# Kernel optimization log

Measured on AMD Instinct MI355X. Metric: run time of the kernel, lower is better.

The kernel has to match this reference:

```python
import jax, jax.numpy as jnp
import numpy as np

P = 3; C = 64; IMG = 48; G = IMG // P
D = C * P * P          # 576 embedding dim == flatten dim
NH = 12; HD = D // NH  # 48 head dim
HID = 4 * D            # 2304
NL = 4; S = G * G      # 256 patches
NQ = 6
QN, QP = -8.0, 7.0     # 4-bit signed LSQ range
EPS = 1e-5


def lsq(w):
    # LSQ fake-quant of weights, step size from LSQ init formula, STE rounding
    alpha = 2.0 * jnp.mean(jnp.abs(w)) / jnp.sqrt(QP)
    q = jnp.clip(w / alpha, QN, QP)
    q = q + jax.lax.stop_gradient(jnp.round(q) - q)
    return q * alpha


def qlinear(x, w, b=None):
    y = x @ lsq(w).T
    return y if b is None else y + b


def ln(x, g, b):
    m = jnp.mean(x, -1, keepdims=True)
    v = jnp.var(x, -1, keepdims=True)
    return (x - m) / jnp.sqrt(v + EPS) * g + b


def mha(q, k, v, in_w, out_w):
    # q,k,v: [S,B,D]; in_w: [3D,D]; out_w: [D,D]; no biases
    Wq, Wk, Wv = jnp.split(lsq(in_w), 3, axis=0)
    def heads(t, W):
        return (t @ W.T).reshape(t.shape[0], t.shape[1], NH, HD)
    qh = heads(q, Wq) * (1.0 / jnp.sqrt(HD))
    kh = heads(k, Wk)
    vh = heads(v, Wv)
    att = jax.nn.softmax(jnp.einsum('qbhd,kbhd->bhqk', qh, kh), axis=-1)
    o = jnp.einsum('bhqk,kbhd->qbhd', att, vh).reshape(q.shape[0], q.shape[1], D)
    return o @ lsq(out_w).T


def _forward(x, lin_enc_w, lin_enc_b, pos_emb, query_embed_w,
             enc_in_w, enc_out_w, enc_l1_w, enc_l1_b, enc_l2_w, enc_l2_b,
             enc_ln1_g, enc_ln1_b, enc_ln2_g, enc_ln2_b,
             dec_sa_in_w, dec_sa_out_w, dec_ca_in_w, dec_ca_out_w,
             dec_l1_w, dec_l1_b, dec_l2_w, dec_l2_b,
             dec_ln1_g, dec_ln1_b, dec_ln2_g, dec_ln2_b, dec_ln3_g, dec_ln3_b,
             head1_w, head1_b, head2_w, head2_b, query_idx):
    B = x.shape[0]
    # unfold -> [S,B,flat], channel-major patch flattening like F.unfold
    t = x.reshape(B, C, G, P, G, P).transpose(0, 1, 3, 5, 2, 4)
    t = t.reshape(B, C * P * P, G * G).transpose(2, 0, 1)  # [S,B,D]
    t = qlinear(t, lin_enc_w, lin_enc_b) + t
    qe = query_embed_w[query_idx].reshape(S, 1, D)   # query_pos, broadcasts over B
    pos = pos_emb[:, None, :]                        # [S,1,D]
    h = t + pos
    for l in range(NL):  # encoder (pre-norm)
        h2 = ln(h, enc_ln1_g[l], enc_ln1_b[l])
        h = h + mha(h2, h2, h2, enc_in_w[l], enc_out_w[l])
        h2 = ln(h, enc_ln2_g[l], enc_ln2_b[l])
        h = h + qlinear(jax.nn.relu(qlinear(h2, enc_l1_w[l], enc_l1_b[l])), enc_l2_w[l], enc_l2_b[l])
    mem = h
    o = mem
    for l in range(NL):  # decoder, memory = encoder output
        o2 = ln(o, dec_ln1_g[l], dec_ln1_b[l])
        qk = o2 + qe
        o = o + mha(qk, qk, o2, dec_sa_in_w[l], dec_sa_out_w[l])
        o2 = ln(o, dec_ln2_g[l], dec_ln2_b[l])
        o = o + mha(o2 + qe, mem, mem, dec_ca_in_w[l], dec_ca_out_w[l])
        o2 = ln(o, dec_ln3_g[l], dec_ln3_b[l])
        o = o + qlinear(jax.nn.relu(qlinear(o2, dec_l1_w[l], dec_l1_b[l])), dec_l2_w[l], dec_l2_b[l])
    # mlp_head with residual
    o = o + qlinear(jax.nn.relu(qlinear(o, head1_w, head1_b)), head2_w, head2_b)
    # fold back: [S,B,D] -> [B,C,IMG,IMG]
    y = o.transpose(1, 2, 0).reshape(B, C, P, P, G, G).transpose(0, 1, 4, 2, 5, 3)
    return y.reshape(B, C, IMG, IMG)


def setup_inputs() -> dict:
    key = jax.random.key(0)
    ks = iter(jax.random.split(key, 64))
    def w(shape):
        return jax.random.normal(next(ks), shape, jnp.float32) * 0.02
    B = 4
    inp = {
        'x': jax.random.normal(next(ks), (B, C, IMG, IMG), jnp.float32),
        'lin_enc_w': w((D, D)), 'lin_enc_b': jnp.zeros((D,), jnp.float32),
        'pos_emb': w((S, D)),
        'query_embed_w': w((NQ, S * D)),
        'enc_in_w': w((NL, 3 * D, D)), 'enc_out_w': w((NL, D, D)),
        'enc_l1_w': w((NL, HID, D)), 'enc_l1_b': jnp.zeros((NL, HID), jnp.float32),
        'enc_l2_w': w((NL, D, HID)), 'enc_l2_b': jnp.zeros((NL, D), jnp.float32),
        'enc_ln1_g': jnp.ones((NL, D), jnp.float32), 'enc_ln1_b': jnp.zeros((NL, D), jnp.float32),
        'enc_ln2_g': jnp.ones((NL, D), jnp.float32), 'enc_ln2_b': jnp.zeros((NL, D), jnp.float32),
        'dec_sa_in_w': w((NL, 3 * D, D)), 'dec_sa_out_w': w((NL, D, D)),
        'dec_ca_in_w': w((NL, 3 * D, D)), 'dec_ca_out_w': w((NL, D, D)),
        'dec_l1_w': w((NL, HID, D)), 'dec_l1_b': jnp.zeros((NL, HID), jnp.float32),
        'dec_l2_w': w((NL, D, HID)), 'dec_l2_b': jnp.zeros((NL, D), jnp.float32),
        'dec_ln1_g': jnp.ones((NL, D), jnp.float32), 'dec_ln1_b': jnp.zeros((NL, D), jnp.float32),
        'dec_ln2_g': jnp.ones((NL, D), jnp.float32), 'dec_ln2_b': jnp.zeros((NL, D), jnp.float32),
        'dec_ln3_g': jnp.ones((NL, D), jnp.float32), 'dec_ln3_b': jnp.zeros((NL, D), jnp.float32),
        'head1_w': w((HID, D)), 'head1_b': jnp.zeros((HID,), jnp.float32),
        'head2_w': w((D, HID)), 'head2_b': jnp.zeros((D,), jnp.float32),
        'query_idx': 0,
    }
    return inp


def reference(x, lin_enc_w, lin_enc_b, pos_emb, query_embed_w,
              enc_in_w, enc_out_w, enc_l1_w, enc_l1_b, enc_l2_w, enc_l2_b,
              enc_ln1_g, enc_ln1_b, enc_ln2_g, enc_ln2_b,
              dec_sa_in_w, dec_sa_out_w, dec_ca_in_w, dec_ca_out_w,
              dec_l1_w, dec_l1_b, dec_l2_w, dec_l2_b,
              dec_ln1_g, dec_ln1_b, dec_ln2_g, dec_ln2_b, dec_ln3_g, dec_ln3_b,
              head1_w, head1_b, head2_w, head2_b, query_idx):
    return _forward(x, lin_enc_w, lin_enc_b, pos_emb, query_embed_w,
                    enc_in_w, enc_out_w, enc_l1_w, enc_l1_b, enc_l2_w, enc_l2_b,
                    enc_ln1_g, enc_ln1_b, enc_ln2_g, enc_ln2_b,
                    dec_sa_in_w, dec_sa_out_w, dec_ca_in_w, dec_ca_out_w,
                    dec_l1_w, dec_l1_b, dec_l2_w, dec_l2_b,
                    dec_ln1_g, dec_ln1_b, dec_ln2_g, dec_ln2_b, dec_ln3_g, dec_ln3_b,
                    head1_w, head1_b, head2_w, head2_b, query_idx)
```

## Files before the change

kernel.cpp:

```cpp
#include <hip/hip_runtime.h>
#include <cstddef>

#define Pp    3
#define Cc    64
#define IMGi  48
#define Gg    16
#define Dd    576
#define NHh   12
#define HDd   48
#define HIDh  2304
#define NLl   4
#define Ss    256
#define Bb    4
#define Mm    1024
#define EPSf  1e-5f
#define NJOBS 43
#define NSTAT 20

typedef short short8 __attribute__((ext_vector_type(8)));
typedef short short4v __attribute__((ext_vector_type(4)));
typedef float f32x4  __attribute__((ext_vector_type(4)));

struct QJobs { const float* ptr[NJOBS]; int n[NJOBS]; int off[NJOBS]; };

__device__ __forceinline__ short f2bf(float f) {
  unsigned u = __float_as_uint(f);
  u = u + 0x7fffu + ((u >> 16) & 1u);
  return (short)(u >> 16);
}

typedef __attribute__((address_space(3))) unsigned lds_u32;
typedef __attribute__((address_space(1))) const unsigned glob_u32;
__device__ __forceinline__ void gload_lds16(const void* g, void* l) {
  __builtin_amdgcn_global_load_lds((glob_u32*)g, (lds_u32*)l, 16, 0, 0);
}


__global__ void k_zero(float* p, int n) {
  int i = blockIdx.x * blockDim.x + threadIdx.x;
  if (i < n) p[i] = 0.f;
}

__global__ void k_abssum(QJobs jobs, float* absum) {
  int job = blockIdx.x >> 6, blk = blockIdx.x & 63;
  const float4* p4 = (const float4*)jobs.ptr[job];
  int n4 = jobs.n[job] >> 2;
  float s0 = 0.f, s1 = 0.f, s2 = 0.f, s3 = 0.f;
  for (int i = blk * 1024 + threadIdx.x; i < n4; i += 64 * 1024) {
    float4 v = p4[i];
    s0 += fabsf(v.x) + fabsf(v.y) + fabsf(v.z) + fabsf(v.w);
    int i1 = i + 256;
    if (i1 < n4) { float4 w = p4[i1]; s1 += fabsf(w.x) + fabsf(w.y) + fabsf(w.z) + fabsf(w.w); }
    int i2 = i + 512;
    if (i2 < n4) { float4 w = p4[i2]; s2 += fabsf(w.x) + fabsf(w.y) + fabsf(w.z) + fabsf(w.w); }
    int i3 = i + 768;
    if (i3 < n4) { float4 w = p4[i3]; s3 += fabsf(w.x) + fabsf(w.y) + fabsf(w.z) + fabsf(w.w); }
  }
  float s = (s0 + s1) + (s2 + s3);
  #pragma unroll
  for (int o = 32; o; o >>= 1) s += __shfl_xor(s, o);
  __shared__ float red[4];
  if ((threadIdx.x & 63) == 0) red[threadIdx.x >> 6] = s;
  __syncthreads();
  if (threadIdx.x == 0) atomicAdd(&absum[job], (red[0] + red[1]) + (red[2] + red[3]));
}

__global__ void k_alpha(QJobs jobs, const float* absum, float* alpha, float* inva) {
  int j = threadIdx.x;
  if (j < NJOBS) {
    float a = 2.f * (absum[j] / (float)jobs.n[j]) / sqrtf(7.f);
    alpha[j] = a;
    inva[j] = 1.f / a;
  }
}

__global__ void k_quant(QJobs jobs, const float* __restrict__ inva, short* __restrict__ wq) {
  int job = blockIdx.x >> 7, blk = blockIdx.x & 127;
  const float* p = jobs.ptr[job];
  int n8 = jobs.n[job] >> 3;
  short* dst = wq + (size_t)jobs.off[job];
  float ia = inva[job];
  for (int i = blk * 512 + threadIdx.x; i < n8; i += 128 * 512) {
    const float4* p4 = (const float4*)(p + (size_t)i * 8);
    float4 w0 = p4[0], w1 = p4[1];
    int i1 = i + 256;
    float4 w2, w3;
    bool has2 = i1 < n8;
    if (has2) { const float4* q4 = (const float4*)(p + (size_t)i1 * 8); w2 = q4[0]; w3 = q4[1]; }
    short8 bv;
    bv[0] = f2bf(rintf(fminf(7.f, fmaxf(-8.f, w0.x * ia))));
    bv[1] = f2bf(rintf(fminf(7.f, fmaxf(-8.f, w0.y * ia))));
    bv[2] = f2bf(rintf(fminf(7.f, fmaxf(-8.f, w0.z * ia))));
    bv[3] = f2bf(rintf(fminf(7.f, fmaxf(-8.f, w0.w * ia))));
    bv[4] = f2bf(rintf(fminf(7.f, fmaxf(-8.f, w1.x * ia))));
    bv[5] = f2bf(rintf(fminf(7.f, fmaxf(-8.f, w1.y * ia))));
    bv[6] = f2bf(rintf(fminf(7.f, fmaxf(-8.f, w1.z * ia))));
    bv[7] = f2bf(rintf(fminf(7.f, fmaxf(-8.f, w1.w * ia))));
    *(short8*)(dst + (size_t)i * 8) = bv;
    if (has2) {
      short8 cv;
      cv[0] = f2bf(rintf(fminf(7.f, fmaxf(-8.f, w2.x * ia))));
      cv[1] = f2bf(rintf(fminf(7.f, fmaxf(-8.f, w2.y * ia))));
      cv[2] = f2bf(rintf(fminf(7.f, fmaxf(-8.f, w2.z * ia))));
      cv[3] = f2bf(rintf(fminf(7.f, fmaxf(-8.f, w2.w * ia))));
      cv[4] = f2bf(rintf(fminf(7.f, fmaxf(-8.f, w3.x * ia))));
      cv[5] = f2bf(rintf(fminf(7.f, fmaxf(-8.f, w3.y * ia))));
      cv[6] = f2bf(rintf(fminf(7.f, fmaxf(-8.f, w3.z * ia))));
      cv[7] = f2bf(rintf(fminf(7.f, fmaxf(-8.f, w3.w * ia))));
      *(short8*)(dst + (size_t)i1 * 8) = cv;
    }
  }
}

__global__ void k_patchify(const float* __restrict__ x, float* __restrict__ t) {
  int i = blockIdx.x * 256 + threadIdx.x;
  if (i >= Mm * Dd) return;
  int d = i % Dd, row = i / Dd;
  int b = row % Bb, s = row / Bb;
  int c = d / 9, r = d % 9;
  int p1 = r / 3, p2 = r % 3;
  int g1 = s / Gg, g2 = s % Gg;
  t[i] = x[((size_t)(b * Cc + c) * IMGi + (g1 * Pp + p1)) * IMGi + (g2 * Pp + p2)];
}

__global__ void k_unpatch(const float* __restrict__ h, float* __restrict__ out) {
  int i = blockIdx.x * 256 + threadIdx.x;
  if (i >= Bb * Cc * IMGi * IMGi) return;
  int j = i % IMGi, t = i / IMGi;
  int r = t % IMGi; t /= IMGi;
  int c = t % Cc;
  int b = t / Cc;
  int g1 = r / Pp, p1 = r % Pp, g2 = j / Pp, p2 = j % Pp;
  int s = g1 * Gg + g2;
  int d = c * 9 + p1 * 3 + p2;
  out[i] = h[(size_t)(s * Bb + b) * Dd + d];
}

#define MT 64
#define NT 64
#define KC 288
#define LDKA 296
#define LDKB 304
#define BCHUNKS 38

__device__ __forceinline__ int bswz(int row, int colByte) {
  return row * (LDKB * 2) + (colByte ^ (((row >> 2) & 3) << 4));
}

__global__ __launch_bounds__(256)
void k_gemm_mfma(const float* __restrict__ Xa, const float* __restrict__ Xb,
                 int n_split, int ldx,
                 const float* __restrict__ qe, const int* __restrict__ qidx,
                 const float* __restrict__ lng, const float* __restrict__ lnb,
                 const float* __restrict__ statA, const float* __restrict__ statB,
                 const float* __restrict__ Wraw, const short* __restrict__ Wq,
                 const float* __restrict__ bias, const float* __restrict__ pos,
                 const float* res, int ldr,
                 float* out, int ldo, float* out2, float* statOut,
                 int N, int K,
                 const float* __restrict__ alpha_p, const float* __restrict__ inva_p,
                 int slot, int relu)
{
  __shared__ short As[MT][LDKA];
  __shared__ short Bs[NT * LDKB];
  const int tid  = threadIdx.x;
  const int wave = tid >> 6, lane = tid & 63;
  const int quad = lane >> 4, l15 = lane & 15;
  const int tile_m = blockIdx.y * MT, tile_n = blockIdx.x * NT;
  const int m_off = (wave >> 1) * 32, n_off = (wave & 1) * 32;
  const int sr = tid >> 2;
  const int sc = (tid & 3) * 8;
  const float inva = inva_p[slot];

  const bool isA = (!Xb || tile_n < n_split);
  const float* X = isA ? Xa : Xb;
  const bool addqe = (qe != nullptr) && isA;
  const float* stat = isA ? statA : statB;
  size_t qe_off = 0;
  if (addqe) qe_off = (size_t)qidx[0] * ((size_t)Ss * Dd);

  float mean = 0.f, sinv = 1.f;
  if (stat) {
    float2 st = *(const float2*)&stat[2 * (tile_m + sr)];
    mean = st.x * (1.f / (float)Dd);
    float var = st.y * (1.f / (float)Dd) - mean * mean;
    sinv = rsqrtf(var + EPSf);
  }

  f32x4 acc00 = {0,0,0,0}, acc01 = {0,0,0,0}, acc10 = {0,0,0,0}, acc11 = {0,0,0,0};

  for (int kc = 0; kc < K; kc += KC) {
    if (Wq) {
      #pragma unroll
      for (int j = 0; j < 10; ++j) {
        const int c = wave * 10 + j;
        if (c < BCHUNKS) {
          const int p = c * 512 + lane * 8;
          const int prow = p / LDKB;
          const int pcolB = (p % LDKB) * 2;
          const int lcolB = pcolB ^ (((prow >> 2) & 3) << 4);
          const short* src = (lcolB < 576)
            ? Wq + (size_t)(tile_n + prow) * K + kc + (lcolB >> 1)
            : Wq;
          gload_lds16(src, (char*)Bs + c * 1024);
        }
      }
    } else {
      const float* wr = Wraw + (size_t)(tile_n + sr) * K + kc;
      #pragma unroll
      for (int j = 0; j < 9; ++j) {
        const int k = sc + j * 32;
        float4 w0 = *(const float4*)(wr + k);
        float4 w1 = *(const float4*)(wr + k + 4);
        short8 bv;
        bv[0] = f2bf(rintf(fminf(7.f, fmaxf(-8.f, w0.x * inva))));
        bv[1] = f2bf(rintf(fminf(7.f, fmaxf(-8.f, w0.y * inva))));
        bv[2] = f2bf(rintf(fminf(7.f, fmaxf(-8.f, w0.z * inva))));
        bv[3] = f2bf(rintf(fminf(7.f, fmaxf(-8.f, w0.w * inva))));
        bv[4] = f2bf(rintf(fminf(7.f, fmaxf(-8.f, w1.x * inva))));
        bv[5] = f2bf(rintf(fminf(7.f, fmaxf(-8.f, w1.y * inva))));
        bv[6] = f2bf(rintf(fminf(7.f, fmaxf(-8.f, w1.z * inva))));
        bv[7] = f2bf(rintf(fminf(7.f, fmaxf(-8.f, w1.w * inva))));
        *(short8*)((char*)Bs + bswz(sr, k * 2)) = bv;
      }
    }

    {
      const int arow = tile_m + sr;
      const float* ar = X + (size_t)arow * ldx + kc;
      const float* qr = addqe ? (qe + qe_off + (size_t)(arow >> 2) * Dd + kc) : nullptr;
      #pragma unroll
      for (int j = 0; j < 9; ++j) {
        const int k = sc + j * 32;
        float4 a0 = *(const float4*)(ar + k);
        float4 a1 = *(const float4*)(ar + k + 4);
        if (stat) {
          float4 g0 = *(const float4*)(lng + kc + k);
          float4 g1 = *(const float4*)(lng + kc + k + 4);
          float4 b0 = *(const float4*)(lnb + kc + k);
          float4 b1 = *(const float4*)(lnb + kc + k + 4);
          a0.x = (a0.x - mean) * sinv * g0.x + b0.x;
          a0.y = (a0.y - mean) * sinv * g0.y + b0.y;
          a0.z = (a0.z - mean) * sinv * g0.z + b0.z;
          a0.w = (a0.w - mean) * sinv * g0.w + b0.w;
          a1.x = (a1.x - mean) * sinv * g1.x + b1.x;
          a1.y = (a1.y - mean) * sinv * g1.y + b1.y;
          a1.z = (a1.z - mean) * sinv * g1.z + b1.z;
          a1.w = (a1.w - mean) * sinv * g1.w + b1.w;
        }
        if (addqe) {
          float4 q0 = *(const float4*)(qr + k);
          float4 q1 = *(const float4*)(qr + k + 4);
          a0.x += q0.x; a0.y += q0.y; a0.z += q0.z; a0.w += q0.w;
          a1.x += q1.x; a1.y += q1.y; a1.z += q1.z; a1.w += q1.w;
        }
        short8 av;
        av[0] = f2bf(a0.x); av[1] = f2bf(a0.y); av[2] = f2bf(a0.z); av[3] = f2bf(a0.w);
        av[4] = f2bf(a1.x); av[5] = f2bf(a1.y); av[6] = f2bf(a1.z); av[7] = f2bf(a1.w);
        *(short8*)&As[sr][k] = av;
      }
    }
    __syncthreads();

    #pragma unroll 3
    for (int ks = 0; ks < KC / 32; ++ks) {
      const int kb = ks * 32 + quad * 8;
      short8 af0 = *(short8*)&As[m_off + l15][kb];
      short8 af1 = *(short8*)&As[m_off + 16 + l15][kb];
      short8 bf0 = *(const short8*)((const char*)Bs + bswz(n_off + l15, kb * 2));
      short8 bf1 = *(const short8*)((const char*)Bs + bswz(n_off + 16 + l15, kb * 2));
      acc00 = __builtin_amdgcn_mfma_f32_16x16x32_bf16(af0, bf0, acc00, 0, 0, 0);
      acc01 = __builtin_amdgcn_mfma_f32_16x16x32_bf16(af0, bf1, acc01, 0, 0, 0);
      acc10 = __builtin_amdgcn_mfma_f32_16x16x32_bf16(af1, bf0, acc10, 0, 0, 0);
      acc11 = __builtin_amdgcn_mfma_f32_16x16x32_bf16(af1, bf1, acc11, 0, 0, 0);
    }
    __syncthreads();
  }

  const float a_s = alpha_p[slot];
  const int rowb = tile_m + m_off + quad * 4;
  const int colb = tile_n + n_off + l15;
  f32x4 accs[4] = {acc00, acc01, acc10, acc11};
  float vsum[2][4], vsq[2][4];
  #pragma unroll
  for (int rt = 0; rt < 2; ++rt)
    #pragma unroll
    for (int r = 0; r < 4; ++r) { vsum[rt][r] = 0.f; vsq[rt][r] = 0.f; }

  #pragma unroll
  for (int t = 0; t < 4; ++t) {
    int row0 = rowb + ((t >> 1) * 16);
    int col  = colb + ((t & 1) * 16);
    float bv = bias ? bias[col] : 0.f;
    #pragma unroll
    for (int r = 0; r < 4; ++r) {
      int row = row0 + r;
      float v = accs[t][r] * a_s + bv;
      if (res) v += res[(size_t)row * ldr + col];
      if (pos) v += pos[(size_t)(row >> 2) * Dd + col];
      if (relu) v = fmaxf(v, 0.f);
      out[(size_t)row * ldo + col] = v;
      if (out2) out2[(size_t)row * ldo + col] = v;
      vsum[t >> 1][r] += v;
      vsq[t >> 1][r]  += v * v;
    }
  }

  if (statOut) {
    #pragma unroll
    for (int rt = 0; rt < 2; ++rt) {
      #pragma unroll
      for (int r = 0; r < 4; ++r) {
        float s = vsum[rt][r], q = vsq[rt][r];
        #pragma unroll
        for (int o = 1; o < 16; o <<= 1) {
          s += __shfl_xor(s, o);
          q += __shfl_xor(q, o);
        }
        if (l15 == 0) {
          int row = rowb + rt * 16 + r;
          atomicAdd(&statOut[2 * row],     s);
          atomicAdd(&statOut[2 * row + 1], q);
        }
      }
    }
  }
}

__global__ __launch_bounds__(256)
void k_attn(const float* __restrict__ QKV, float* __restrict__ ctx, float scale) {
  __shared__ short Ks[256][72];
  __shared__ short Qs[64][72];
  __shared__ short Vt[48][264];
  __shared__ short Pq[64][264];
  const int qt = blockIdx.x;
  const int b  = blockIdx.y / NHh, h = blockIdx.y % NHh;
  const int tid = threadIdx.x;
  const int w = tid >> 6, lane = tid & 63, quad = lane >> 4, l15 = lane & 15;

  {
    const float* kp = QKV + (size_t)(tid * Bb + b) * 1728 + Dd + h * HDd;
    #pragma unroll
    for (int d0 = 0; d0 < 48; d0 += 4) {
      float4 f = *(const float4*)(kp + d0);
      short4v v = { f2bf(f.x), f2bf(f.y), f2bf(f.z), f2bf(f.w) };
      *(short4v*)&Ks[tid][d0] = v;
    }
    short4v z = {0, 0, 0, 0};
    *(short4v*)&Ks[tid][48] = z; *(short4v*)&Ks[tid][52] = z;
    *(short4v*)&Ks[tid][56] = z; *(short4v*)&Ks[tid][60] = z;
    const float* vp = QKV + (size_t)(tid * Bb + b) * 1728 + 2 * Dd + h * HDd;
    #pragma unroll
    for (int d0 = 0; d0 < 48; d0 += 4) {
      float4 f = *(const float4*)(vp + d0);
      Vt[d0 + 0][tid] = f2bf(f.x);
      Vt[d0 + 1][tid] = f2bf(f.y);
      Vt[d0 + 2][tid] = f2bf(f.z);
      Vt[d0 + 3][tid] = f2bf(f.w);
    }
    if (tid < 64) {
      const float* qp = QKV + (size_t)((qt * 64 + tid) * Bb + b) * 1728 + h * HDd;
      #pragma unroll
      for (int d0 = 0; d0 < 48; d0 += 4) {
        float4 f = *(const float4*)(qp + d0);
        short4v v = { f2bf(f.x), f2bf(f.y), f2bf(f.z), f2bf(f.w) };
        *(short4v*)&Qs[tid][d0] = v;
      }
      *(short4v*)&Qs[tid][48] = z; *(short4v*)&Qs[tid][52] = z;
      *(short4v*)&Qs[tid][56] = z; *(short4v*)&Qs[tid][60] = z;
    }
  }
  __syncthreads();

  short8 bq0 = *(short8*)&Qs[w * 16 + l15][quad * 8];
  short8 bq1 = *(short8*)&Qs[w * 16 + l15][32 + quad * 8];
  f32x4 sf[16];
  #pragma unroll
  for (int mt = 0; mt < 16; ++mt) {
    f32x4 acc = {0, 0, 0, 0};
    short8 a0 = *(short8*)&Ks[mt * 16 + l15][quad * 8];
    short8 a1 = *(short8*)&Ks[mt * 16 + l15][32 + quad * 8];
    acc = __builtin_amdgcn_mfma_f32_16x16x32_bf16(a0, bq0, acc, 0, 0, 0);
    acc = __builtin_amdgcn_mfma_f32_16x16x32_bf16(a1, bq1, acc, 0, 0, 0);
    sf[mt] = acc;
  }

  float mx = -1e30f;
  #pragma unroll
  for (int mt = 0; mt < 16; ++mt)
    #pragma unroll
    for (int r = 0; r < 4; ++r) {
      sf[mt][r] *= scale;
      mx = fmaxf(mx, sf[mt][r]);
    }
  mx = fmaxf(mx, __shfl_xor(mx, 16));
  mx = fmaxf(mx, __shfl_xor(mx, 32));
  float sum = 0.f;
  #pragma unroll
  for (int mt = 0; mt < 16; ++mt)
    #pragma unroll
    for (int r = 0; r < 4; ++r) {
      float e = __expf(sf[mt][r] - mx);
      sf[mt][r] = e;
      sum += e;
    }
  sum += __shfl_xor(sum, 16);
  sum += __shfl_xor(sum, 32);
  float inv = 1.f / sum;

  #pragma unroll
  for (int mt = 0; mt < 16; ++mt) {
    short4v p = { f2bf(sf[mt][0] * inv), f2bf(sf[mt][1] * inv),
                  f2bf(sf[mt][2] * inv), f2bf(sf[mt][3] * inv) };
    *(short4v*)&Pq[w * 16 + l15][mt * 16 + quad * 4] = p;
  }
  __syncthreads();

  f32x4 of0 = {0,0,0,0}, of1 = {0,0,0,0}, of2 = {0,0,0,0};
  #pragma unroll
  for (int kt = 0; kt < 8; ++kt) {
    short8 a = *(short8*)&Pq[w * 16 + l15][kt * 32 + quad * 8];
    short8 b0 = *(short8*)&Vt[l15][kt * 32 + quad * 8];
    short8 b1 = *(short8*)&Vt[16 + l15][kt * 32 + quad * 8];
    short8 b2 = *(short8*)&Vt[32 + l15][kt * 32 + quad * 8];
    of0 = __builtin_amdgcn_mfma_f32_16x16x32_bf16(a, b0, of0, 0, 0, 0);
    of1 = __builtin_amdgcn_mfma_f32_16x16x32_bf16(a, b1, of1, 0, 0, 0);
    of2 = __builtin_amdgcn_mfma_f32_16x16x32_bf16(a, b2, of2, 0, 0, 0);
  }
  const int qg = qt * 64 + w * 16 + quad * 4;
  #pragma unroll
  for (int r = 0; r < 4; ++r) {
    float* cr = ctx + (size_t)((qg + r) * Bb + b) * Dd + h * HDd + l15;
    cr[0]  = of0[r];
    cr[16] = of1[r];
    cr[32] = of2[r];
  }
}


extern "C" void kernel_launch(void* const* d_in, const int* in_sizes, int n_in,
                              void* d_out, int out_size, void* d_ws, size_t ws_size,
                              hipStream_t stream) {
  (void)in_sizes; (void)n_in; (void)out_size;
  const float* x            = (const float*)d_in[0];
  const float* lin_enc_w    = (const float*)d_in[1];
  const float* lin_enc_b    = (const float*)d_in[2];
  const float* pos_emb      = (const float*)d_in[3];
  const float* query_embed  = (const float*)d_in[4];
  const float* enc_in_w     = (const float*)d_in[5];
  const float* enc_out_w    = (const float*)d_in[6];
  const float* enc_l1_w     = (const float*)d_in[7];
  const float* enc_l1_b     = (const float*)d_in[8];
  const float* enc_l2_w     = (const float*)d_in[9];
  const float* enc_l2_b     = (const float*)d_in[10];
  const float* enc_ln1_g    = (const float*)d_in[11];
  const float* enc_ln1_b    = (const float*)d_in[12];
  const float* enc_ln2_g    = (const float*)d_in[13];
  const float* enc_ln2_b    = (const float*)d_in[14];
  const float* dec_sa_in_w  = (const float*)d_in[15];
  const float* dec_sa_out_w = (const float*)d_in[16];
  const float* dec_ca_in_w  = (const float*)d_in[17];
  const float* dec_ca_out_w = (const float*)d_in[18];
  const float* dec_l1_w     = (const float*)d_in[19];
  const float* dec_l1_b     = (const float*)d_in[20];
  const float* dec_l2_w     = (const float*)d_in[21];
  const float* dec_l2_b     = (const float*)d_in[22];
  const float* dec_ln1_g    = (const float*)d_in[23];
  const float* dec_ln1_b    = (const float*)d_in[24];
  const float* dec_ln2_g    = (const float*)d_in[25];
  const float* dec_ln2_b    = (const float*)d_in[26];
  const float* dec_ln3_g    = (const float*)d_in[27];
  const float* dec_ln3_b    = (const float*)d_in[28];
  const float* head1_w      = (const float*)d_in[29];
  const float* head1_b      = (const float*)d_in[30];
  const float* head2_w      = (const float*)d_in[31];
  const float* head2_b      = (const float*)d_in[32];
  const int*   query_idx    = (const int*)d_in[33];
  float* out = (float*)d_out;

  const int DD  = Dd * Dd;
  const int IN3 = 3 * Dd * Dd;
  const int FF  = HIDh * Dd;
  const int MD  = Mm * Dd;

  float* ws = (float*)d_ws;
  float* ABSUM = ws;
  float* ALPHA = ws + 64;
  float* INVA  = ws + 128;
  float* STAT  = ws + 256;
  const int STATF = NSTAT * Mm * 2;
  float* H   = STAT + STATF;
  float* MEM = H   + MD;
  float* SCR = MEM + MD;
  float* CTX = SCR + MD;
  float* QKV = CTX + MD;
  size_t act_floats = 256 + (size_t)STATF + 4 * (size_t)MD + (size_t)Mm * HIDh;
  short* WQ = (short*)(ws + act_floats);
  const size_t WQ_ELEMS = (size_t)DD + 4 * ((size_t)IN3 + DD + FF + FF)
                        + 4 * ((size_t)IN3 + DD + IN3 + DD + FF + FF)
                        + 2 * (size_t)FF;
  const bool use_wq = ws_size >= act_floats * 4 + WQ_ELEMS * 2;

  auto T = [&](int i) { return STAT + (size_t)i * (Mm * 2); };

  QJobs jobs;
  int j = 0; int off = 0;
  auto addjob = [&](const float* p, int n) { jobs.ptr[j] = p; jobs.n[j] = n; jobs.off[j] = off; off += n; j++; };
  addjob(lin_enc_w, DD);
  for (int l = 0; l < NLl; ++l) addjob(enc_in_w  + (size_t)l * IN3, IN3);
  for (int l = 0; l < NLl; ++l) addjob(enc_out_w + (size_t)l * DD,  DD);
  for (int l = 0; l < NLl; ++l) addjob(enc_l1_w  + (size_t)l * FF,  FF);
  for (int l = 0; l < NLl; ++l) addjob(enc_l2_w  + (size_t)l * FF,  FF);
  for (int l = 0; l < NLl; ++l) addjob(dec_sa_in_w  + (size_t)l * IN3, IN3);
  for (int l = 0; l < NLl; ++l) addjob(dec_sa_out_w + (size_t)l * DD,  DD);
  for (int l = 0; l < NLl; ++l) addjob(dec_ca_in_w  + (size_t)l * IN3, IN3);
  for (int l = 0; l < NLl; ++l) addjob(dec_ca_out_w + (size_t)l * DD,  DD);
  for (int l = 0; l < NLl; ++l) addjob(dec_l1_w + (size_t)l * FF, FF);
  for (int l = 0; l < NLl; ++l) addjob(dec_l2_w + (size_t)l * FF, FF);
  addjob(head1_w, FF);
  addjob(head2_w, FF);

  const int ZN = 256 + STATF;
  k_zero<<<(ZN + 255) / 256, 256, 0, stream>>>(ws, ZN);
  k_abssum<<<NJOBS * 64, 256, 0, stream>>>(jobs, ABSUM);
  k_alpha<<<1, 64, 0, stream>>>(jobs, ABSUM, ALPHA, INVA);
  if (use_wq) k_quant<<<NJOBS * 128, 256, 0, stream>>>(jobs, INVA, WQ);

  auto gemm = [&](const float* Xa, const float* Xb, int n_split, int ldx,
                  const float* qe, const float* lng, const float* lnb,
                  const float* statA, const float* statB,
                  const float* W, int slot, const float* bias, const float* pos,
                  const float* res, int ldr,
                  float* o, int ldo, float* o2, float* statOut,
                  int N, int K, int relu) {
    dim3 grid(N / NT, Mm / MT);
    const short* wq = use_wq ? WQ + (size_t)jobs.off[slot] : nullptr;
    const float* wr = use_wq ? nullptr : W;
    k_gemm_mfma<<<grid, 256, 0, stream>>>(Xa, Xb, n_split, ldx, qe, query_idx,
                                          lng, lnb, statA, statB,
                                          wr, wq, bias, pos, res, ldr,
                                          o, ldo, o2, statOut,
                                          N, K, ALPHA, INVA, slot, relu);
  };

  const float scale = 1.f / sqrtf((float)HDd);
  auto attn = [&](const float* out_w, int out_slot, float* statOut) {
    k_attn<<<dim3(Ss / 64, Bb * NHh), 256, 0, stream>>>(QKV, CTX, scale);
    gemm(CTX, nullptr, 0, Dd, nullptr, nullptr, nullptr, nullptr, nullptr,
         out_w, out_slot, nullptr, nullptr, H, Dd, H, Dd, nullptr, statOut,
         Dd, Dd, 0);
  };

  const int NELEM = Mm * Dd;
  const int EB = (NELEM + 255) / 256;

  k_patchify<<<EB, 256, 0, stream>>>(x, SCR);
  gemm(SCR, nullptr, 0, Dd, nullptr, nullptr, nullptr, nullptr, nullptr,
       lin_enc_w, 0, lin_enc_b, pos_emb, SCR, Dd, H, Dd, nullptr, T(0),
       Dd, Dd, 0);

  for (int l = 0; l < NLl; ++l) {
    gemm(H, nullptr, 0, Dd, nullptr, enc_ln1_g + l * Dd, enc_ln1_b + l * Dd,
         T(2 * l), nullptr,
         enc_in_w + (size_t)l * IN3, 1 + l,
         nullptr, nullptr, nullptr, 0, QKV, 1728, nullptr, nullptr, 1728, Dd, 0);
    attn(enc_out_w + (size_t)l * DD, 5 + l, T(2 * l + 1));
    gemm(H, nullptr, 0, Dd, nullptr, enc_ln2_g + l * Dd, enc_ln2_b + l * Dd,
         T(2 * l + 1), nullptr,
         enc_l1_w + (size_t)l * FF, 9 + l,
         enc_l1_b + l * HIDh, nullptr, nullptr, 0, QKV, HIDh, nullptr, nullptr,
         HIDh, Dd, 1);
    gemm(QKV, nullptr, 0, HIDh, nullptr, nullptr, nullptr, nullptr, nullptr,
         enc_l2_w + (size_t)l * FF, 13 + l,
         enc_l2_b + l * Dd, nullptr, H, Dd, H, Dd,
         (l == NLl - 1) ? MEM : nullptr, T(2 * l + 2), Dd, HIDh, 0);
  }

  for (int l = 0; l < NLl; ++l) {
    float* ln1s = T(8 + 3 * l);
    gemm(H, H, 2 * Dd, Dd, query_embed,
         dec_ln1_g + l * Dd, dec_ln1_b + l * Dd, ln1s, ln1s,
         dec_sa_in_w + (size_t)l * IN3, 17 + l,
         nullptr, nullptr, nullptr, 0, QKV, 1728, nullptr, nullptr, 1728, Dd, 0);
    attn(dec_sa_out_w + (size_t)l * DD, 21 + l, T(9 + 3 * l));
    gemm(H, MEM, Dd, Dd, query_embed,
         dec_ln2_g + l * Dd, dec_ln2_b + l * Dd, T(9 + 3 * l), nullptr,
         dec_ca_in_w + (size_t)l * IN3, 25 + l,
         nullptr, nullptr, nullptr, 0, QKV, 1728, nullptr, nullptr, 1728, Dd, 0);
    attn(dec_ca_out_w + (size_t)l * DD, 29 + l, T(10 + 3 * l));
    gemm(H, nullptr, 0, Dd, nullptr, dec_ln3_g + l * Dd, dec_ln3_b + l * Dd,
         T(10 + 3 * l), nullptr,
         dec_l1_w + (size_t)l * FF, 33 + l,
         dec_l1_b + l * HIDh, nullptr, nullptr, 0, QKV, HIDh, nullptr, nullptr,
         HIDh, Dd, 1);
    gemm(QKV, nullptr, 0, HIDh, nullptr, nullptr, nullptr, nullptr, nullptr,
         dec_l2_w + (size_t)l * FF, 37 + l,
         dec_l2_b + l * Dd, nullptr, H, Dd, H, Dd, nullptr,
         (l < NLl - 1) ? T(11 + 3 * l) : nullptr, Dd, HIDh, 0);
  }

  gemm(H, nullptr, 0, Dd, nullptr, nullptr, nullptr, nullptr, nullptr,
       head1_w, 41, head1_b, nullptr, nullptr, 0, QKV, HIDh, nullptr, nullptr,
       HIDh, Dd, 1);
  gemm(QKV, nullptr, 0, HIDh, nullptr, nullptr, nullptr, nullptr, nullptr,
       head2_w, 42, head2_b, nullptr, H, Dd, H, Dd, nullptr, nullptr,
       Dd, HIDh, 0);

  k_unpatch<<<EB, 256, 0, stream>>>(H, out);
}
```

Measured before the change: 1.531 ms.

## Store intermediate activations in bf16 and stage GEMM A-tiles asynchronously into LDS

Activations consumed as GEMM inputs (hidden state, QKV, FFN hidden, attention context, encoder memory) are now written in bf16 alongside or instead of fp32. This halves the global traffic for these buffers and removes the per-element fp32-to-bf16 conversion in the GEMM A-load and in attention staging. When no LayerNorm or query-embedding add is needed, the A tile is loaded with direct global-to-LDS async copies using the same swizzled layout as B. Residual paths keep fp32 copies, but LayerNorm inputs are now read from bf16, which adds rounding error before normalization.

After: 1.330 ms. 1.15x faster.

```diff
diff --git a/kernel.cpp b/kernel.cpp
--- a/kernel.cpp
+++ b/kernel.cpp
@@ -20,6 +20,7 @@
 typedef short short8 __attribute__((ext_vector_type(8)));
 typedef short short4v __attribute__((ext_vector_type(4)));
 typedef float f32x4  __attribute__((ext_vector_type(4)));
+typedef unsigned short ushort_t;
 
 struct QJobs { const float* ptr[NJOBS]; int n[NJOBS]; int off[NJOBS]; };
 
@@ -27,6 +28,9 @@
   unsigned u = __float_as_uint(f);
   u = u + 0x7fffu + ((u >> 16) & 1u);
   return (short)(u >> 16);
+}
+__device__ __forceinline__ float bf2f(short s) {
+  return __uint_as_float(((unsigned)(unsigned short)s) << 16);
 }
 
 typedef __attribute__((address_space(3))) unsigned lds_u32;
@@ -112,7 +116,8 @@
   }
 }
 
-__global__ void k_patchify(const float* __restrict__ x, float* __restrict__ t) {
+__global__ void k_patchify(const float* __restrict__ x, float* __restrict__ t,
+                           ushort_t* __restrict__ tb) {
   int i = blockIdx.x * 256 + threadIdx.x;
   if (i >= Mm * Dd) return;
   int d = i % Dd, row = i / Dd;
@@ -120,7 +125,9 @@
   int c = d / 9, r = d % 9;
   int p1 = r / 3, p2 = r % 3;
   int g1 = s / Gg, g2 = s % Gg;
-  t[i] = x[((size_t)(b * Cc + c) * IMGi + (g1 * Pp + p1)) * IMGi + (g2 * Pp + p2)];
+  float v = x[((size_t)(b * Cc + c) * IMGi + (g1 * Pp + p1)) * IMGi + (g2 * Pp + p2)];
+  t[i] = v;
+  tb[i] = (ushort_t)f2bf(v);
 }
 
 __global__ void k_unpatch(const float* __restrict__ h, float* __restrict__ out) {
@@ -139,7 +146,6 @@
 #define MT 64
 #define NT 64
 #define KC 288
-#define LDKA 296
 #define LDKB 304
 #define BCHUNKS 38
 
@@ -147,8 +153,26 @@
   return row * (LDKB * 2) + (colByte ^ (((row >> 2) & 3) << 4));
 }
 
+__device__ __forceinline__ void stage_async(const ushort_t* base, int ld,
+                                            char* lds, int wave, int lane) {
+  #pragma unroll
+  for (int j = 0; j < 10; ++j) {
+    const int c = wave * 10 + j;
+    if (c < BCHUNKS) {
+      const int p = c * 512 + lane * 8;
+      const int prow = p / LDKB;
+      const int pcol2 = (p % LDKB) * 2;
+      const int lcol = pcol2 ^ (((prow >> 2) & 3) << 4);
+      const ushort_t* src = (lcol < 576)
+        ? base + (size_t)prow * ld + (lcol >> 1)
+        : base;
+      gload_lds16(src, lds + c * 1024);
+    }
+  }
+}
+
 __global__ __launch_bounds__(256)
-void k_gemm_mfma(const float* __restrict__ Xa, const float* __restrict__ Xb,
+void k_gemm_mfma(const ushort_t* __restrict__ Xa, const ushort_t* __restrict__ Xb,
                  int n_split, int ldx,
                  const float* __restrict__ qe, const int* __restrict__ qidx,
                  const float* __restrict__ lng, const float* __restrict__ lnb,
@@ -156,12 +180,13 @@
                  const float* __restrict__ Wraw, const short* __restrict__ Wq,
                  const float* __restrict__ bias, const float* __restrict__ pos,
                  const float* res, int ldr,
-                 float* out, int ldo, float* out2, float* statOut,
+                 float* out, int ldo,
+                 ushort_t* outbf, ushort_t* outbf2, float* statOut,
                  int N, int K,
                  const float* __restrict__ alpha_p, const float* __restrict__ inva_p,
                  int slot, int relu)
 {
-  __shared__ short As[MT][LDKA];
+  __shared__ short As[NT * LDKB];
   __shared__ short Bs[NT * LDKB];
   const int tid  = threadIdx.x;
   const int wave = tid >> 6, lane = tid & 63;
@@ -173,9 +198,10 @@
   const float inva = inva_p[slot];
 
   const bool isA = (!Xb || tile_n < n_split);
-  const float* X = isA ? Xa : Xb;
+  const ushort_t* X = isA ? Xa : Xb;
   const bool addqe = (qe != nullptr) && isA;
   const float* stat = isA ? statA : statB;
+  const bool a_reg = (stat != nullptr) || addqe;
   size_t qe_off = 0;
   if (addqe) qe_off = (size_t)qidx[0] * ((size_t)Ss * Dd);
 
@@ -191,20 +217,8 @@
 
   for (int kc = 0; kc < K; kc += KC) {
     if (Wq) {
-      #pragma unroll
-      for (int j = 0; j < 10; ++j) {
-        const int c = wave * 10 + j;
-        if (c < BCHUNKS) {
-          const int p = c * 512 + lane * 8;
-          const int prow = p / LDKB;
-          const int pcolB = (p % LDKB) * 2;
-          const int lcolB = pcolB ^ (((prow >> 2) & 3) << 4);
-          const short* src = (lcolB < 576)
-            ? Wq + (size_t)(tile_n + prow) * K + kc + (lcolB >> 1)
-            : Wq;
-          gload_lds16(src, (char*)Bs + c * 1024);
-        }
-      }
+      stage_async((const ushort_t*)Wq + (size_t)tile_n * K + kc, K,
+                  (char*)Bs, wave, lane);
     } else {
       const float* wr = Wraw + (size_t)(tile_n + sr) * K + kc;
       #pragma unroll
@@ -225,39 +239,43 @@
       }
     }
 
-    {
+    if (!a_reg) {
+      stage_async(X + (size_t)tile_m * ldx + kc, ldx, (char*)As, wave, lane);
+    } else {
       const int arow = tile_m + sr;
-      const float* ar = X + (size_t)arow * ldx + kc;
+      const ushort_t* xr = X + (size_t)arow * ldx + kc;
       const float* qr = addqe ? (qe + qe_off + (size_t)(arow >> 2) * Dd + kc) : nullptr;
       #pragma unroll
       for (int j = 0; j < 9; ++j) {
         const int k = sc + j * 32;
-        float4 a0 = *(const float4*)(ar + k);
-        float4 a1 = *(const float4*)(ar + k + 4);
+        short8 xv = *(const short8*)(xr + k);
+        float a[8];
+        #pragma unroll
+        for (int e = 0; e < 8; ++e) a[e] = bf2f(xv[e]);
         if (stat) {
           float4 g0 = *(const float4*)(lng + kc + k);
           float4 g1 = *(const float4*)(lng + kc + k + 4);
           float4 b0 = *(const float4*)(lnb + kc + k);
           float4 b1 = *(const float4*)(lnb + kc + k + 4);
-          a0.x = (a0.x - mean) * sinv * g0.x + b0.x;
-          a0.y = (a0.y - mean) * sinv * g0.y + b0.y;
-          a0.z = (a0.z - mean) * sinv * g0.z + b0.z;
-          a0.w = (a0.w - mean) * sinv * g0.w + b0.w;
-          a1.x = (a1.x - mean) * sinv * g1.x + b1.x;
-          a1.y = (a1.y - mean) * sinv * g1.y + b1.y;
-          a1.z = (a1.z - mean) * sinv * g1.z + b1.z;
-          a1.w = (a1.w - mean) * sinv * g1.w + b1.w;
+          a[0] = (a[0] - mean) * sinv * g0.x + b0.x;
+          a[1] = (a[1] - mean) * sinv * g0.y + b0.y;
+          a[2] = (a[2] - mean) * sinv * g0.z + b0.z;
+          a[3] = (a[3] - mean) * sinv * g0.w + b0.w;
+          a[4] = (a[4] - mean) * sinv * g1.x + b1.x;
+          a[5] = (a[5] - mean) * sinv * g1.y + b1.y;
+          a[6] = (a[6] - mean) * sinv * g1.z + b1.z;
+          a[7] = (a[7] - mean) * sinv * g1.w + b1.w;
         }
         if (addqe) {
           float4 q0 = *(const float4*)(qr + k);
           float4 q1 = *(const float4*)(qr + k + 4);
-          a0.x += q0.x; a0.y += q0.y; a0.z += q0.z; a0.w += q0.w;
-          a1.x += q1.x; a1.y += q1.y; a1.z += q1.z; a1.w += q1.w;
+          a[0] += q0.x; a[1] += q0.y; a[2] += q0.z; a[3] += q0.w;
+          a[4] += q1.x; a[5] += q1.y; a[6] += q1.z; a[7] += q1.w;
         }
         short8 av;
-        av[0] = f2bf(a0.x); av[1] = f2bf(a0.y); av[2] = f2bf(a0.z); av[3] = f2bf(a0.w);
-        av[4] = f2bf(a1.x); av[5] = f2bf(a1.y); av[6] = f2bf(a1.z); av[7] = f2bf(a1.w);
-        *(short8*)&As[sr][k] = av;
+        #pragma unroll
+        for (int e = 0; e < 8; ++e) av[e] = f2bf(a[e]);
+        *(short8*)((char*)As + bswz(sr, k * 2)) = av;
       }
     }
     __syncthreads();
@@ -265,8 +283,8 @@
     #pragma unroll 3
     for (int ks = 0; ks < KC / 32; ++ks) {
       const int kb = ks * 32 + quad * 8;
-      short8 af0 = *(short8*)&As[m_off + l15][kb];
-      short8 af1 = *(short8*)&As[m_off + 16 + l15][kb];
+      short8 af0 = *(const short8*)((const char*)As + bswz(m_off + l15, kb * 2));
+      short8 af1 = *(const short8*)((const char*)As + bswz(m_off + 16 + l15, kb * 2));
       short8 bf0 = *(const short8*)((const char*)Bs + bswz(n_off + l15, kb * 2));
       short8 bf1 = *(const short8*)((const char*)Bs + bswz(n_off + 16 + l15, kb * 2));
       acc00 = __builtin_amdgcn_mfma_f32_16x16x32_bf16(af0, bf0, acc00, 0, 0, 0);
@@ -299,8 +317,9 @@
       if (res) v += res[(size_t)row * ldr + col];
       if (pos) v += pos[(size_t)(row >> 2) * Dd + col];
       if (relu) v = fmaxf(v, 0.f);
-      out[(size_t)row * ldo + col] = v;
-      if (out2) out2[(size_t)row * ldo + col] = v;
+      if (out)    out[(size_t)row * ldo + col] = v;
+      if (outbf)  outbf[(size_t)row * ldo + col]  = (ushort_t)f2bf(v);
+      if (outbf2) outbf2[(size_t)row * ldo + col] = (ushort_t)f2bf(v);
       vsum[t >> 1][r] += v;
       vsq[t >> 1][r]  += v * v;
     }
@@ -328,7 +347,7 @@
 }
 
 __global__ __launch_bounds__(256)
-void k_attn(const float* __restrict__ QKV, float* __restrict__ ctx, float scale) {
+void k_attn(const ushort_t* __restrict__ QKV, ushort_t* __restrict__ ctx, float scale) {
   __shared__ short Ks[256][72];
   __shared__ short Qs[64][72];
   __shared__ short Vt[48][264];
@@ -339,33 +358,25 @@
   const int w = tid >> 6, lane = tid & 63, quad = lane >> 4, l15 = lane & 15;
 
   {
-    const float* kp = QKV + (size_t)(tid * Bb + b) * 1728 + Dd + h * HDd;
+    const ushort_t* kp = QKV + (size_t)(tid * Bb + b) * 1728 + Dd + h * HDd;
     #pragma unroll
-    for (int d0 = 0; d0 < 48; d0 += 4) {
-      float4 f = *(const float4*)(kp + d0);
-      short4v v = { f2bf(f.x), f2bf(f.y), f2bf(f.z), f2bf(f.w) };
-      *(short4v*)&Ks[tid][d0] = v;
-    }
+    for (int d0 = 0; d0 < 48; d0 += 8)
+      *(short8*)&Ks[tid][d0] = *(const short8*)(kp + d0);
     short4v z = {0, 0, 0, 0};
     *(short4v*)&Ks[tid][48] = z; *(short4v*)&Ks[tid][52] = z;
     *(short4v*)&Ks[tid][56] = z; *(short4v*)&Ks[tid][60] = z;
-    const float* vp = QKV + (size_t)(tid * Bb + b) * 1728 + 2 * Dd + h * HDd;
+    const ushort_t* vp = QKV + (size_t)(tid * Bb + b) * 1728 + 2 * Dd + h * HDd;
     #pragma unroll
-    for (int d0 = 0; d0 < 48; d0 += 4) {
-      float4 f = *(const float4*)(vp + d0);
-      Vt[d0 + 0][tid] = f2bf(f.x);
-      Vt[d0 + 1][tid] = f2bf(f.y);
-      Vt[d0 + 2][tid] = f2bf(f.z);
-      Vt[d0 + 3][tid] = f2bf(f.w);
+    for (int d0 = 0; d0 < 48; d0 += 8) {
+      short8 v = *(const short8*)(vp + d0);
+      #pragma unroll
+      for (int e = 0; e < 8; ++e) Vt[d0 + e][tid] = v[e];
     }
     if (tid < 64) {
-      const float* qp = QKV + (size_t)((qt * 64 + tid) * Bb + b) * 1728 + h * HDd;
+      const ushort_t* qp = QKV + (size_t)((qt * 64 + tid) * Bb + b) * 1728 + h * HDd;
       #pragma unroll
-      for (int d0 = 0; d0 < 48; d0 += 4) {
-        float4 f = *(const float4*)(qp + d0);
-        short4v v = { f2bf(f.x), f2bf(f.y), f2bf(f.z), f2bf(f.w) };
-        *(short4v*)&Qs[tid][d0] = v;
-      }
+      for (int d0 = 0; d0 < 48; d0 += 8)
+        *(short8*)&Qs[tid][d0] = *(const short8*)(qp + d0);
       *(short4v*)&Qs[tid][48] = z; *(short4v*)&Qs[tid][52] = z;
       *(short4v*)&Qs[tid][56] = z; *(short4v*)&Qs[tid][60] = z;
     }
@@ -430,10 +441,10 @@
   const int qg = qt * 64 + w * 16 + quad * 4;
   #pragma unroll
   for (int r = 0; r < 4; ++r) {
-    float* cr = ctx + (size_t)((qg + r) * Bb + b) * Dd + h * HDd + l15;
-    cr[0]  = of0[r];
-    cr[16] = of1[r];
-    cr[32] = of2[r];
+    ushort_t* cr = ctx + (size_t)((qg + r) * Bb + b) * Dd + h * HDd + l15;
+    cr[0]  = (ushort_t)f2bf(of0[r]);
+    cr[16] = (ushort_t)f2bf(of1[r]);
+    cr[32] = (ushort_t)f2bf(of2[r]);
   }
 }
 
@@ -490,16 +501,19 @@
   float* STAT  = ws + 256;
   const int STATF = NSTAT * Mm * 2;
   float* H   = STAT + STATF;
-  float* MEM = H   + MD;
-  float* SCR = MEM + MD;
-  float* CTX = SCR + MD;
-  float* QKV = CTX + MD;
-  size_t act_floats = 256 + (size_t)STATF + 4 * (size_t)MD + (size_t)Mm * HIDh;
-  short* WQ = (short*)(ws + act_floats);
+  float* SCR = H + MD;
+  ushort_t* Hb   = (ushort_t*)(SCR + MD);
+  ushort_t* SCRb = Hb + MD;
+  ushort_t* MEMb = SCRb + MD;
+  ushort_t* CTXb = MEMb + MD;
+  ushort_t* QKVb = CTXb + MD;
+  size_t act_bytes = (256 + (size_t)STATF + 2 * (size_t)MD) * 4
+                   + (4 * (size_t)MD + (size_t)Mm * HIDh) * 2;
+  short* WQ = (short*)(QKVb + (size_t)Mm * HIDh);
   const size_t WQ_ELEMS = (size_t)DD + 4 * ((size_t)IN3 + DD + FF + FF)
                         + 4 * ((size_t)IN3 + DD + IN3 + DD + FF + FF)
                         + 2 * (size_t)FF;
-  const bool use_wq = ws_size >= act_floats * 4 + WQ_ELEMS * 2;
+  const bool use_wq = ws_size >= act_bytes + WQ_ELEMS * 2;
 
   auto T = [&](int i) { return STAT + (size_t)i * (Mm * 2); };
 
@@ -526,85 +540,90 @@
   k_alpha<<<1, 64, 0, stream>>>(jobs, ABSUM, ALPHA, INVA);
   if (use_wq) k_quant<<<NJOBS * 128, 256, 0, stream>>>(jobs, INVA, WQ);
 
-  auto gemm = [&](const float* Xa, const float* Xb, int n_split, int ldx,
+  auto gemm = [&](const ushort_t* Xa, const ushort_t* Xb, int n_split, int ldx,
                   const float* qe, const float* lng, const float* lnb,
                   const float* statA, const float* statB,
                   const float* W, int slot, const float* bias, const float* pos,
                   const float* res, int ldr,
-                  float* o, int ldo, float* o2, float* statOut,
-                  int N, int K, int relu) {
+                  float* o, int ldo, ushort_t* obf, ushort_t* obf2,
+                  float* statOut, int N, int K, int relu) {
     dim3 grid(N / NT, Mm / MT);
     const short* wq = use_wq ? WQ + (size_t)jobs.off[slot] : nullptr;
     const float* wr = use_wq ? nullptr : W;
     k_gemm_mfma<<<grid, 256, 0, stream>>>(Xa, Xb, n_split, ldx, qe, query_idx,
                                           lng, lnb, statA, statB,
                                           wr, wq, bias, pos, res, ldr,
-                                          o, ldo, o2, statOut,
+                                          o, ldo, obf, obf2, statOut,
                                           N, K, ALPHA, INVA, slot, relu);
   };
 
   const float scale = 1.f / sqrtf((float)HDd);
   auto attn = [&](const float* out_w, int out_slot, float* statOut) {
-    k_attn<<<dim3(Ss / 64, Bb * NHh), 256, 0, stream>>>(QKV, CTX, scale);
-    gemm(CTX, nullptr, 0, Dd, nullptr, nullptr, nullptr, nullptr, nullptr,
-         out_w, out_slot, nullptr, nullptr, H, Dd, H, Dd, nullptr, statOut,
-         Dd, Dd, 0);
+    k_attn<<<dim3(Ss / 64, Bb * NHh), 256, 0, stream>>>(QKVb, CTXb, scale);
+    gemm(CTXb, nullptr, 0, Dd, nullptr, nullptr, nullptr, nullptr, nullptr,
+         out_w, out_slot, nullptr, nullptr, H, Dd,
+         H, Dd, Hb, nullptr, statOut, Dd, Dd, 0);
   };
 
   const int NELEM = Mm * Dd;
   const int EB = (NELEM + 255) / 256;
 
-  k_patchify<<<EB, 256, 0, stream>>>(x, SCR);
-  gemm(SCR, nullptr, 0, Dd, nullptr, nullptr, nullptr, nullptr, nullptr,
-       lin_enc_w, 0, lin_enc_b, pos_emb, SCR, Dd, H, Dd, nullptr, T(0),
-       Dd, Dd, 0);
+  k_patchify<<<EB, 256, 0, stream>>>(x, SCR, SCRb);
+  gemm(SCRb, nullptr, 0, Dd, nullptr, nullptr, nullptr, nullptr, nullptr,
+       lin_enc_w, 0, lin_enc_b, pos_emb, SCR, Dd,
+       H, Dd, Hb, nullptr, T(0), Dd, Dd, 0);
 
   for (int l = 0; l < NLl; ++l) {
-    gemm(H, nullptr, 0, Dd, nullptr, enc_ln1_g + l * Dd, enc_ln1_b + l * Dd,
+    gemm(Hb, nullptr, 0, Dd, nullptr, enc_ln1_g + l * Dd, enc_ln1_b + l * Dd,
          T(2 * l), nullptr,
          enc_in_w + (size_t)l * IN3, 1 + l,
-         nullptr, nullptr, nullptr, 0, QKV, 1728, nullptr, nullptr, 1728, Dd, 0);
+         nullptr, nullptr, nullptr, 0,
+         nullptr, 1728, QKVb, nullptr, nullptr, 1728, Dd, 0);
     attn(enc_out_w + (size_t)l * DD, 5 + l, T(2 * l + 1));
-    gemm(H, nullptr, 0, Dd, nullptr, enc_ln2_g + l * Dd, enc_ln2_b + l * Dd,
+    gemm(Hb, nullptr, 0, Dd, nullptr, enc_ln2_g + l * Dd, enc_ln2_b + l * Dd,
          T(2 * l + 1), nullptr,
          enc_l1_w + (size_t)l * FF, 9 + l,
-         enc_l1_b + l * HIDh, nullptr, nullptr, 0, QKV, HIDh, nullptr, nullptr,
-         HIDh, Dd, 1);
-    gemm(QKV, nullptr, 0, HIDh, nullptr, nullptr, nullptr, nullptr, nullptr,
+         enc_l1_b + l * HIDh, nullptr, nullptr, 0,
+         nullptr, HIDh, QKVb, nullptr, nullptr, HIDh, Dd, 1);
+    gemm(QKVb, nullptr, 0, HIDh, nullptr, nullptr, nullptr, nullptr, nullptr,
          enc_l2_w + (size_t)l * FF, 13 + l,
-         enc_l2_b + l * Dd, nullptr, H, Dd, H, Dd,
-         (l == NLl - 1) ? MEM : nullptr, T(2 * l + 2), Dd, HIDh, 0);
+         enc_l2_b + l * Dd, nullptr, H, Dd,
+         H, Dd, Hb, (l == NLl - 1) ? MEMb : nullptr, T(2 * l + 2),
+         Dd, HIDh, 0);
   }
 
   for (int l = 0; l < NLl; ++l) {
     float* ln1s = T(8 + 3 * l);
-    gemm(H, H, 2 * Dd, Dd, query_embed,
+    gemm(Hb, Hb, 2 * Dd, Dd, query_embed,
          dec_ln1_g + l * Dd, dec_ln1_b + l * Dd, ln1s, ln1s,
          dec_sa_in_w + (size_t)l * IN3, 17 + l,
-         nullptr, nullptr, nullptr, 0, QKV, 1728, nullptr, nullptr, 1728, Dd, 0);
+         nullptr, nullptr, nullptr, 0,
+         nullptr, 1728, QKVb, nullptr, nullptr, 1728, Dd, 0);
     attn(dec_sa_out_w + (size_t)l * DD, 21 + l, T(9 + 3 * l));
-    gemm(H, MEM, Dd, Dd, query_embed,
+    gemm(Hb, MEMb, Dd, Dd, query_embed,
          dec_ln2_g + l * Dd, dec_ln2_b + l * Dd, T(9 + 3 * l), nullptr,
          dec_ca_in_w + (size_t)l * IN3, 25 + l,
-         nullptr, nullptr, nullptr, 0, QKV, 1728, nullptr, nullptr, 1728, Dd, 0);
+         nullptr, nullptr, nullptr, 0,
+         nullptr, 1728, QKVb, nullptr, nullptr, 1728, Dd, 0);
     attn(dec_ca_out_w + (size_t)l * DD, 29 + l, T(10 + 3 * l));
-    gemm(H, nullptr, 0, Dd, nullptr, dec_ln3_g + l * Dd, dec_ln3_b + l * Dd,
+    gemm(Hb, nullptr, 0, Dd, nullptr, dec_ln3_g + l * Dd, dec_ln3_b + l * Dd,
          T(10 + 3 * l), nullptr,
          dec_l1_w + (size_t)l * FF, 33 + l,
-         dec_l1_b + l * HIDh, nullptr, nullptr, 0, QKV, HIDh, nullptr, nullptr,
-         HIDh, Dd, 1);
-    gemm(QKV, nullptr, 0, HIDh, nullptr, nullptr, nullptr, nullptr, nullptr,
+         dec_l1_b + l * HIDh, nullptr, nullptr, 0,
+         nullptr, HIDh, QKVb, nullptr, nullptr, HIDh, Dd, 1);
+    gemm(QKVb, nullptr, 0, HIDh, nullptr, nullptr, nullptr, nullptr, nullptr,
          dec_l2_w + (size_t)l * FF, 37 + l,
-         dec_l2_b + l * Dd, nullptr, H, Dd, H, Dd, nullptr,
-         (l < NLl - 1) ? T(11 + 3 * l) : nullptr, Dd, HIDh, 0);
-  }
-
-  gemm(H, nullptr, 0, Dd, nullptr, nullptr, nullptr, nullptr, nullptr,
-       head1_w, 41, head1_b, nullptr, nullptr, 0, QKV, HIDh, nullptr, nullptr,
-       HIDh, Dd, 1);
-  gemm(QKV, nullptr, 0, HIDh, nullptr, nullptr, nullptr, nullptr, nullptr,
-       head2_w, 42, head2_b, nullptr, H, Dd, H, Dd, nullptr, nullptr,
-       Dd, HIDh, 0);
+         dec_l2_b + l * Dd, nullptr, H, Dd,
+         H, Dd, Hb, nullptr, (l < NLl - 1) ? T(11 + 3 * l) : nullptr,
+         Dd, HIDh, 0);
+  }
+
+  gemm(Hb, nullptr, 0, Dd, nullptr, nullptr, nullptr, nullptr, nullptr,
+       head1_w, 41, head1_b, nullptr, nullptr, 0,
+       nullptr, HIDh, QKVb, nullptr, nullptr, HIDh, Dd, 1);
+  gemm(QKVb, nullptr, 0, HIDh, nullptr, nullptr, nullptr, nullptr, nullptr,
+       head2_w, 42, head2_b, nullptr, H, Dd,
+       H, Dd, nullptr, nullptr, nullptr, Dd, HIDh, 0);
 
   k_unpatch<<<EB, 256, 0, stream>>>(H, out);
 }
```
